# Performance work log

Hardware: AMD Instinct MI355X
Metric: run time of the kernel (lower is better)

## Reference

```python
import jax, jax.numpy as jnp
import numpy as np
import math

MODEL_DIM = 1024
B, S = 4, 2048


def setup_inputs() -> dict:
    key = jax.random.key(0)
    k_x, k_q, k_k, k_v = jax.random.split(key, 4)
    r5 = math.sqrt(5)
    x = jax.random.normal(k_x, (B, S, MODEL_DIM), dtype=jnp.float32)
    Q = jax.random.uniform(k_q, (MODEL_DIM, MODEL_DIM), minval=-r5, maxval=r5, dtype=jnp.float32)
    K = jax.random.uniform(k_k, (MODEL_DIM, MODEL_DIM), minval=-r5, maxval=r5, dtype=jnp.float32)
    V = jax.random.uniform(k_v, (MODEL_DIM, MODEL_DIM), minval=-r5, maxval=r5, dtype=jnp.float32)
    # attention_input == 'both' -> a == model_dim -> F is the full identity
    F = jnp.eye(MODEL_DIM, dtype=jnp.float32)
    return {"x": x, "Q": Q, "K": K, "V": V, "F": F}


def reference(x, Q, K, V, F):
    d = x.shape[-1]
    xf = jnp.matmul(x, F)
    Qx = jnp.matmul(xf, Q)          # [B,S,D]
    Kx = jnp.matmul(xf, K)          # [B,S,D]
    Vx = jnp.matmul(x, V)           # [B,S,D]
    scores = jnp.einsum('bqd,bkd->bqk', Qx, Kx) / math.sqrt(d)  # [B,S,S]
    seq = x.shape[1]
    mask = jnp.triu(jnp.ones((seq, seq), dtype=bool), k=1)
    scores = jnp.where(mask, -jnp.inf, scores)
    probs = jax.nn.softmax(scores, axis=-1)
    out = jnp.matmul(probs, Vx)     # [B,S,D]
    return (out, probs)
```

## Files before the change

kernel.cpp:

```cpp
#include <hip/hip_runtime.h>
#include <hip/hip_fp16.h>

typedef _Float16 f16;
typedef __attribute__((ext_vector_type(8))) _Float16 f16x8;
typedef __attribute__((ext_vector_type(4))) _Float16 f16x4;
typedef __attribute__((ext_vector_type(4))) float    f32x4;

#define D_MODEL 1024
#define SEQ     2048
#define BATCH   4
#define M_TOT   (BATCH * SEQ)
#define NE      ((long)M_TOT * D_MODEL)
#define WE      ((long)D_MODEL * D_MODEL)
#define OUT_ELEMS  ((long)M_TOT * D_MODEL)

static __device__ __forceinline__ f16x8 frag_read(const f16* lds, int row, int c)
{
    const f16x8* L = (const f16x8*)lds;
    return L[row * 4 + (c ^ ((row >> 1) & 3))];
}

static __device__ __forceinline__ void stage_tile(const f16* __restrict__ g, int row0,
                                                  int ld, int k0, f16* ldsbase,
                                                  int wave, int lane)
{
#pragma unroll
    for (int j = 0; j < 2; ++j) {
        const int chunk = wave * 2 + j;
        const int off16 = chunk * 64 + lane;
        const int row   = off16 >> 2;
        const int slot  = (off16 & 3) ^ ((row >> 1) & 3);
        const f16* src = g + (long)(row0 + row) * ld + (k0 + slot * 8);
        f16* dst = ldsbase + chunk * 512;
        __builtin_amdgcn_global_load_lds((const __attribute__((address_space(1))) void*)src,
                                         (__attribute__((address_space(3))) void*)dst,
                                         16, 0, 0);
    }
}

template<int ROWS>
static __device__ __forceinline__ void stage8(const f16* __restrict__ g, int row0,
                                              int ld, int k0, f16* dstbase,
                                              int wave, int lane)
{
#pragma unroll
    for (int j = 0; j < ROWS / 128; ++j) {
        const int off16 = j * 512 + wave * 64 + lane;
        const int row   = off16 >> 2;
        const int slot  = (off16 & 3) ^ ((row >> 1) & 3);
        const f16* src = g + (long)(row0 + row) * ld + (k0 + slot * 8);
        f16* dst = dstbase + (j * 512 + wave * 64) * 8;
        __builtin_amdgcn_global_load_lds((const __attribute__((address_space(1))) void*)src,
                                         (__attribute__((address_space(3))) void*)dst,
                                         16, 0, 0);
    }
}

template<int DUAL> struct G8 {
    static constexpr int BUF    = DUAL ? 24576 : 12288;
    static constexpr int OFF_AL = 8192;
    static constexpr int OFF_BH = DUAL ? 16384 : 8192;
    static constexpr int OFF_BL = 20480;
};

template<int DUAL>
static __device__ __forceinline__ void g8_issueA(const f16* Ah, const f16* Al, int ld,
                                                 int m0, f16* lds, int t, int wave, int lane)
{
    f16* b = lds + (t & 1) * G8<DUAL>::BUF;
    stage8<256>(Ah, m0, ld, t * 32, b, wave, lane);
    if constexpr (DUAL) stage8<256>(Al, m0, ld, t * 32, b + G8<DUAL>::OFF_AL, wave, lane);
}
template<int DUAL>
static __device__ __forceinline__ void g8_issueBh(const f16* BTh, int ld, int n0,
                                                  f16* lds, int t, int wave, int lane)
{
    stage8<128>(BTh, n0, ld, t * 32, lds + (t & 1) * G8<DUAL>::BUF + G8<DUAL>::OFF_BH, wave, lane);
}
template<int DUAL>
static __device__ __forceinline__ void g8_issueBl(const f16* BTl, int ld, int n0,
                                                  f16* lds, int t, int wave, int lane)
{
    stage8<128>(BTl, n0, ld, t * 32, lds + (t & 1) * G8<DUAL>::BUF + G8<DUAL>::OFF_BL, wave, lane);
}

template<int DUAL>
static __device__ __forceinline__ void gemm8_pipe(
    const f16* __restrict__ Ah, const f16* __restrict__ Al,
    const f16* __restrict__ BTh, const f16* __restrict__ BTl,
    int ld, int m0, int n0, int nT, f16* lds, f32x4 acc[4][4], int wave, int lane)
{
    const int wr = wave >> 1, wc = wave & 1;
    const int cf = lane >> 4;

#pragma unroll
    for (int mi = 0; mi < 4; ++mi)
#pragma unroll
        for (int ni = 0; ni < 4; ++ni) acc[mi][ni] = (f32x4){0.f, 0.f, 0.f, 0.f};

    g8_issueA<DUAL>(Ah, Al, ld, m0, lds, 0, wave, lane);
    g8_issueBh<DUAL>(BTh, ld, n0, lds, 0, wave, lane);
    if constexpr (DUAL) g8_issueBl<DUAL>(BTl, ld, n0, lds, 0, wave, lane);
    g8_issueA<DUAL>(Ah, Al, ld, m0, lds, 1, wave, lane);
    g8_issueBh<DUAL>(BTh, ld, n0, lds, 1, wave, lane);

    for (int t = 0; t < nT; ++t) {
        if (t < nT - 1) {
            if constexpr (DUAL) {
                g8_issueBl<DUAL>(BTl, ld, n0, lds, t + 1, wave, lane);
                asm volatile("s_waitcnt vmcnt(6)" ::: "memory");
            } else {
                asm volatile("s_waitcnt vmcnt(3)" ::: "memory");
            }
        } else {
            asm volatile("s_waitcnt vmcnt(0)" ::: "memory");
        }
        __builtin_amdgcn_sched_barrier(0);
        __builtin_amdgcn_s_barrier();
        __builtin_amdgcn_sched_barrier(0);

        f16* buf = lds + (t & 1) * G8<DUAL>::BUF;
        f16x8 fbh[4], fbl[4], fah[4], fal[4];
#pragma unroll
        for (int i = 0; i < 4; ++i) {
            const int rb = wc * 64 + i * 16 + (lane & 15);
            fbh[i] = frag_read(buf + G8<DUAL>::OFF_BH, rb, cf);
            if constexpr (DUAL) fbl[i] = frag_read(buf + G8<DUAL>::OFF_BL, rb, cf);
        }
#pragma unroll
        for (int i = 0; i < 4; ++i) {
            const int ra = wr * 64 + i * 16 + (lane & 15);
            fah[i] = frag_read(buf, ra, cf);
            if constexpr (DUAL) fal[i] = frag_read(buf + G8<DUAL>::OFF_AL, ra, cf);
        }

        if constexpr (DUAL) {
#pragma unroll
            for (int mi = 0; mi < 4; ++mi)
#pragma unroll
                for (int ni = 0; ni < 4; ++ni)
                    acc[mi][ni] = __builtin_amdgcn_mfma_f32_16x16x32_f16(fah[mi], fbh[ni], acc[mi][ni], 0, 0, 0);
        } else {
#pragma unroll
            for (int mi = 0; mi < 2; ++mi)
#pragma unroll
                for (int ni = 0; ni < 4; ++ni)
                    acc[mi][ni] = __builtin_amdgcn_mfma_f32_16x16x32_f16(fah[mi], fbh[ni], acc[mi][ni], 0, 0, 0);
        }

        asm volatile("s_waitcnt lgkmcnt(0)" ::: "memory");
        __builtin_amdgcn_sched_barrier(0);
        __builtin_amdgcn_s_barrier();
        __builtin_amdgcn_sched_barrier(0);

        if (t + 2 < nT) {
            g8_issueA<DUAL>(Ah, Al, ld, m0, lds, t + 2, wave, lane);
            g8_issueBh<DUAL>(BTh, ld, n0, lds, t + 2, wave, lane);
        }
        __builtin_amdgcn_sched_barrier(0);

        __builtin_amdgcn_s_setprio(1);
        if constexpr (DUAL) {
#pragma unroll
            for (int mi = 0; mi < 4; ++mi) {
#pragma unroll
                for (int ni = 0; ni < 4; ++ni)
                    acc[mi][ni] = __builtin_amdgcn_mfma_f32_16x16x32_f16(fah[mi], fbl[ni], acc[mi][ni], 0, 0, 0);
#pragma unroll
                for (int ni = 0; ni < 4; ++ni)
                    acc[mi][ni] = __builtin_amdgcn_mfma_f32_16x16x32_f16(fal[mi], fbh[ni], acc[mi][ni], 0, 0, 0);
            }
        } else {
#pragma unroll
            for (int mi = 2; mi < 4; ++mi)
#pragma unroll
                for (int ni = 0; ni < 4; ++ni)
                    acc[mi][ni] = __builtin_amdgcn_mfma_f32_16x16x32_f16(fah[mi], fbh[ni], acc[mi][ni], 0, 0, 0);
        }
        __builtin_amdgcn_s_setprio(0);
    }
}

#define BUFE2 32768

static __device__ __forceinline__ void g256_main(const f16* Ah, const f16* Al,
                                                 const f16* BTh, int ld, int m0, int n0,
                                                 f16* lds, int t, int wave, int lane)
{
    f16* b = lds + (t & 1) * BUFE2;
    stage8<256>(Ah,  m0, ld, t * 32, b,         wave, lane);
    stage8<256>(Al,  m0, ld, t * 32, b + 8192,  wave, lane);
    stage8<256>(BTh, n0, ld, t * 32, b + 16384, wave, lane);
}
static __device__ __forceinline__ void g256_bl(const f16* BTl, int ld, int n0,
                                               f16* lds, int t, int wave, int lane)
{
    stage8<256>(BTl, n0, ld, t * 32, lds + (t & 1) * BUFE2 + 24576, wave, lane);
}

static __device__ __forceinline__ void gemm256d(
    const f16* __restrict__ Ah, const f16* __restrict__ Al,
    const f16* __restrict__ BTh, const f16* __restrict__ BTl,
    int ld, int m0, int n0, f16* lds, f32x4 acc[8][4], int wave, int lane)
{
    const int wr = wave >> 2, wc = wave & 3;
    const int cf = lane >> 4;

#pragma unroll
    for (int mi = 0; mi < 8; ++mi)
#pragma unroll
        for (int ni = 0; ni < 4; ++ni) acc[mi][ni] = (f32x4){0.f, 0.f, 0.f, 0.f};

    g256_main(Ah, Al, BTh, ld, m0, n0, lds, 0, wave, lane);
    g256_bl(BTl, ld, n0, lds, 0, wave, lane);
    g256_main(Ah, Al, BTh, ld, m0, n0, lds, 1, wave, lane);

    for (int t = 0; t < 32; ++t) {
        if (t < 31) {
            g256_bl(BTl, ld, n0, lds, t + 1, wave, lane);
            asm volatile("s_waitcnt vmcnt(8)" ::: "memory");
        } else {
            asm volatile("s_waitcnt vmcnt(0)" ::: "memory");
        }
        __builtin_amdgcn_sched_barrier(0);
        __builtin_amdgcn_s_barrier();
        __builtin_amdgcn_sched_barrier(0);

        f16* buf = lds + (t & 1) * BUFE2;
        f16x8 fbh[4], fbl[4], fah[8], fal[8];
#pragma unroll
        for (int ni = 0; ni < 4; ++ni) {
            const int rb = wc * 64 + ni * 16 + (lane & 15);
            fbh[ni] = frag_read(buf + 16384, rb, cf);
            fbl[ni] = frag_read(buf + 24576, rb, cf);
        }
#pragma unroll
        for (int mi = 0; mi < 8; ++mi) {
            const int ra = wr * 128 + mi * 16 + (lane & 15);
            fah[mi] = frag_read(buf,        ra, cf);
            fal[mi] = frag_read(buf + 8192, ra, cf);
        }

#pragma unroll
        for (int mi = 0; mi < 8; ++mi)
#pragma unroll
            for (int ni = 0; ni < 4; ++ni)
                acc[mi][ni] = __builtin_amdgcn_mfma_f32_16x16x32_f16(fah[mi], fbh[ni], acc[mi][ni], 0, 0, 0);

        asm volatile("s_waitcnt lgkmcnt(0)" ::: "memory");
        __builtin_amdgcn_sched_barrier(0);
        __builtin_amdgcn_s_barrier();
        __builtin_amdgcn_sched_barrier(0);

        if (t < 30)
            g256_main(Ah, Al, BTh, ld, m0, n0, lds, t + 2, wave, lane);
        __builtin_amdgcn_sched_barrier(0);

        __builtin_amdgcn_s_setprio(1);
#pragma unroll
        for (int mi = 0; mi < 8; ++mi) {
#pragma unroll
            for (int ni = 0; ni < 4; ++ni)
                acc[mi][ni] = __builtin_amdgcn_mfma_f32_16x16x32_f16(fah[mi], fbl[ni], acc[mi][ni], 0, 0, 0);
#pragma unroll
            for (int ni = 0; ni < 4; ++ni)
                acc[mi][ni] = __builtin_amdgcn_mfma_f32_16x16x32_f16(fal[mi], fbh[ni], acc[mi][ni], 0, 0, 0);
        }
        __builtin_amdgcn_s_setprio(0);
    }
}

__global__ __launch_bounds__(512, 2) void k_gemm_T(
    const f16* __restrict__ xh, const f16* __restrict__ xl,
    const f16* __restrict__ WhT, const f16* __restrict__ WlT,
    f16* __restrict__ Th, f16* __restrict__ Tl)
{
    __shared__ __align__(16) f16 lds[49152];
    const int lane = threadIdx.x & 63, wave = threadIdx.x >> 6;
    const int L = blockIdx.x;
    const int swz = (L & 7) * 32 + (L >> 3);
    const int m0 = (swz >> 3) * 256;
    const int n0 = (swz & 7) * 128;
    f32x4 acc[4][4];
    gemm8_pipe<1>(xh, xl, WhT, WlT, D_MODEL, m0, n0, 32, lds, acc, wave, lane);
    const int wr = wave >> 1, wc = wave & 1;
#pragma unroll
    for (int mi = 0; mi < 4; ++mi)
#pragma unroll
        for (int ni = 0; ni < 4; ++ni) {
            const int gn = n0 + wc * 64 + ni * 16 + (lane & 15);
#pragma unroll
            for (int r = 0; r < 4; ++r) {
                const int gm = m0 + wr * 64 + mi * 16 + (lane >> 4) * 4 + r;
                const float v = acc[mi][ni][r];
                const f16 h = (f16)v;
                Th[(long)gm * D_MODEL + gn] = h;
                Tl[(long)gm * D_MODEL + gn] = (f16)(v - (float)h);
            }
        }
}

__global__ __launch_bounds__(512, 2) void k_mega1(
    const f16* __restrict__ Th, const f16* __restrict__ Tl,
    const f16* __restrict__ xh, const f16* __restrict__ xl,
    const f16* __restrict__ VhT,
    float* __restrict__ scores, f16* __restrict__ VxT)
{
    __shared__ __align__(16) f16 lds[65536];
    const int lane = threadIdx.x & 63, wave = threadIdx.x >> 6;

    if (blockIdx.x < 144) {
        const int L = blockIdx.x;
        const int b = L / 36;
        const int t = L - b * 36;
        int qt = (int)((sqrtf(8.f * (float)t + 1.f) - 1.f) * 0.5f);
        while ((qt + 1) * (qt + 2) / 2 <= t) ++qt;
        while (qt * (qt + 1) / 2 > t) --qt;
        const int kt = t - qt * (qt + 1) / 2;

        const long ob = (long)b * SEQ * D_MODEL;
        f32x4 acc[8][4];
        gemm256d(Th + ob, Tl + ob, xh + ob, xl + ob, D_MODEL,
                 qt * 256, kt * 256, lds, acc, wave, lane);

        float* sb = scores + (long)b * SEQ * SEQ;
        const int wr = wave >> 2, wc = wave & 3;
#pragma unroll
        for (int mi = 0; mi < 8; ++mi)
#pragma unroll
            for (int ni = 0; ni < 4; ++ni) {
                const int k = kt * 256 + wc * 64 + ni * 16 + (lane & 15);
#pragma unroll
                for (int r = 0; r < 4; ++r) {
                    const int q = qt * 256 + wr * 128 + mi * 16 + (lane >> 4) * 4 + r;
                    sb[(long)q * SEQ + k] = acc[mi][ni][r] * 0.03125f;
                }
            }
    } else {
        const int idx = blockIdx.x - 144;
        const int m0 = (idx >> 3) * 256;
        const int n0 = (idx & 7) * 128;
        f32x4 acc[4][4];
        gemm8_pipe<0>(xh, nullptr, VhT, nullptr, D_MODEL, m0, n0, 32, lds, acc, wave, lane);
        const int wr = wave >> 1, wc = wave & 1;
#pragma unroll
        for (int mi = 0; mi < 4; ++mi) {
            const int gm0 = m0 + wr * 64 + mi * 16 + (lane >> 4) * 4;
            const int b = gm0 >> 11, s = gm0 & 2047;
#pragma unroll
            for (int ni = 0; ni < 4; ++ni) {
                const int gn = n0 + wc * 64 + ni * 16 + (lane & 15);
                f16x4 p = {(f16)acc[mi][ni][0], (f16)acc[mi][ni][1],
                           (f16)acc[mi][ni][2], (f16)acc[mi][ni][3]};
                *(f16x4*)(VxT + ((long)b * D_MODEL + gn) * SEQ + s) = p;
            }
        }
    }
}

__global__ __launch_bounds__(512, 4) void k_gemm_pv8(
    const f16* __restrict__ P, const f16* __restrict__ VT, float* __restrict__ out)
{
    __shared__ __align__(16) f16 lds[24576];
    const int lane = threadIdx.x & 63, wave = threadIdx.x >> 6;
    const int i = blockIdx.x;
    const int qt = 7 - (i >> 5);
    const int dt = (i >> 2) & 7;
    const int b  = i & 3;
    const int nT = 8 * (qt + 1);
    f32x4 acc[4][4];
    const f16* Pb  = P  + (long)b * SEQ * SEQ;
    const f16* VTb = VT + (long)b * D_MODEL * SEQ;
    gemm8_pipe<0>(Pb, nullptr, VTb, nullptr, SEQ, qt * 256, dt * 128, nT, lds, acc, wave, lane);
    float* ob = out + (long)b * SEQ * D_MODEL;
    const int wr = wave >> 1, wc = wave & 1;
#pragma unroll
    for (int mi = 0; mi < 4; ++mi)
#pragma unroll
        for (int ni = 0; ni < 4; ++ni) {
            const int d = dt * 128 + wc * 64 + ni * 16 + (lane & 15);
#pragma unroll
            for (int r = 0; r < 4; ++r) {
                const int qq = qt * 256 + wr * 64 + mi * 16 + (lane >> 4) * 4 + r;
                ob[(long)qq * D_MODEL + d] = acc[mi][ni][r];
            }
        }
}

static __device__ __forceinline__ void gemm_core_dual(
    const f16* __restrict__ Ah, const f16* __restrict__ Al,
    const f16* __restrict__ BTh, const f16* __restrict__ BTl,
    int ld, int m0, int n0, int kEnd, f16* lds, f32x4 acc[4][4])
{
    const int t = threadIdx.x;
    const int lane = t & 63;
    const int wave = t >> 6;
    const int wr = wave >> 1, wc = wave & 1;
    const int cfrag = lane >> 4;

#pragma unroll
    for (int mi = 0; mi < 4; ++mi)
#pragma unroll
        for (int ni = 0; ni < 4; ++ni)
            acc[mi][ni] = (f32x4){0.f, 0.f, 0.f, 0.f};

    for (int k0 = 0; k0 < kEnd; k0 += 32) {
        stage_tile(Ah,  m0, ld, k0, lds,         wave, lane);
        stage_tile(BTh, n0, ld, k0, lds + 4096,  wave, lane);
        stage_tile(Al,  m0, ld, k0, lds + 8192,  wave, lane);
        stage_tile(BTl, n0, ld, k0, lds + 12288, wave, lane);
        __syncthreads();

        f16x8 fah[4], fbh[4], fal[4], fbl[4];
#pragma unroll
        for (int i = 0; i < 4; ++i) {
            fah[i] = frag_read(lds,         wr * 64 + i * 16 + (lane & 15), cfrag);
            fbh[i] = frag_read(lds + 4096,  wc * 64 + i * 16 + (lane & 15), cfrag);
            fal[i] = frag_read(lds + 8192,  wr * 64 + i * 16 + (lane & 15), cfrag);
            fbl[i] = frag_read(lds + 12288, wc * 64 + i * 16 + (lane & 15), cfrag);
        }
#pragma unroll
        for (int mi = 0; mi < 4; ++mi)
#pragma unroll
            for (int ni = 0; ni < 4; ++ni) {
                acc[mi][ni] = __builtin_amdgcn_mfma_f32_16x16x32_f16(fah[mi], fbh[ni], acc[mi][ni], 0, 0, 0);
                acc[mi][ni] = __builtin_amdgcn_mfma_f32_16x16x32_f16(fah[mi], fbl[ni], acc[mi][ni], 0, 0, 0);
                acc[mi][ni] = __builtin_amdgcn_mfma_f32_16x16x32_f16(fal[mi], fbh[ni], acc[mi][ni], 0, 0, 0);
            }
        __syncthreads();
    }
}

__global__ __launch_bounds__(256) void k_split_all(
    const float* __restrict__ x, const float* __restrict__ Q,
    const float* __restrict__ K, const float* __restrict__ V,
    f16* __restrict__ xh, f16* __restrict__ xl,
    f16* __restrict__ Qh, f16* __restrict__ Ql,
    f16* __restrict__ Kh, f16* __restrict__ Kl,
    f16* __restrict__ VhT)
{
    __shared__ float tile[32][33];
    const int bid = blockIdx.x;
    if (bid < 2560) {
        const float* src; f16 *dh, *dl; long base;
        if (bid < 2048)      { src = x; dh = xh; dl = xl; base = (long)bid * 4096; }
        else if (bid < 2304) { src = Q; dh = Qh; dl = Ql; base = (long)(bid - 2048) * 4096; }
        else                 { src = K; dh = Kh; dl = Kl; base = (long)(bid - 2304) * 4096; }
#pragma unroll
        for (int j = 0; j < 4; ++j) {
            const long i = base + (j * 256 + threadIdx.x) * 4;
            float4 v = *(const float4*)(src + i);
            f16 h0 = (f16)v.x, h1 = (f16)v.y, h2 = (f16)v.z, h3 = (f16)v.w;
            f16x4 hh = {h0, h1, h2, h3};
            f16x4 ll = {(f16)(v.x - (float)h0), (f16)(v.y - (float)h1),
                        (f16)(v.z - (float)h2), (f16)(v.w - (float)h3)};
            *(f16x4*)(dh + i) = hh;
            *(f16x4*)(dl + i) = ll;
        }
    } else {
        const int idx = bid - 2560;
        const int n0 = (idx & 31) * 32, k0 = (idx >> 5) * 32;
        const int c = threadIdx.x & 31, r8 = threadIdx.x >> 5;
#pragma unroll
        for (int i = 0; i < 4; ++i) {
            const int r = r8 + i * 8;
            tile[r][c] = V[(long)(k0 + r) * D_MODEL + n0 + c];
        }
        __syncthreads();
#pragma unroll
        for (int i = 0; i < 4; ++i) {
            const int r = r8 + i * 8;
            VhT[(long)(n0 + r) * D_MODEL + k0 + c] = (f16)tile[c][r];
        }
    }
}

__global__ __launch_bounds__(256, 2) void k_gemm_w(
    const f16* __restrict__ Qh, const f16* __restrict__ Ql,
    const f16* __restrict__ Kh, const f16* __restrict__ Kl,
    f16* __restrict__ WhT, f16* __restrict__ WlT)
{
    __shared__ __align__(16) f16 lds[16384];
    f32x4 acc[4][4];
    const int m0 = blockIdx.y * 128, n0 = blockIdx.x * 128;
    gemm_core_dual(Qh, Ql, Kh, Kl, D_MODEL, m0, n0, D_MODEL, lds, acc);
    const int lane = threadIdx.x & 63, wave = threadIdx.x >> 6;
    const int wr = wave >> 1, wc = wave & 1;
#pragma unroll
    for (int mi = 0; mi < 4; ++mi)
#pragma unroll
        for (int ni = 0; ni < 4; ++ni) {
            const int gn = n0 + wc * 64 + ni * 16 + (lane & 15);
#pragma unroll
            for (int r = 0; r < 4; ++r) {
                const int gm = m0 + wr * 64 + mi * 16 + (lane >> 4) * 4 + r;
                const float v = acc[mi][ni][r];
                const f16 h = (f16)v;
                WhT[(long)gn * D_MODEL + gm] = h;
                WlT[(long)gn * D_MODEL + gm] = (f16)(v - (float)h);
            }
        }
}

__global__ __launch_bounds__(256) void k_softmax(float* __restrict__ probs,
                                                 f16* __restrict__ probs16)
{
    const long row = blockIdx.x;
    const int q = (int)(row & (SEQ - 1));
    float* s = probs + row * SEQ;
    const int t = threadIdx.x;
    const int kb = t * 8;
    float v[8] = {0.f, 0.f, 0.f, 0.f, 0.f, 0.f, 0.f, 0.f};
    if (kb <= q) {
        float4 u0 = *(const float4*)(s + kb);
        float4 u1 = *(const float4*)(s + kb + 4);
        v[0] = u0.x; v[1] = u0.y; v[2] = u0.z; v[3] = u0.w;
        v[4] = u1.x; v[5] = u1.y; v[6] = u1.z; v[7] = u1.w;
    }
    float mx = -3.0e38f;
#pragma unroll
    for (int j = 0; j < 8; ++j) if (kb + j <= q) mx = fmaxf(mx, v[j]);
#pragma unroll
    for (int off = 32; off > 0; off >>= 1) mx = fmaxf(mx, __shfl_xor(mx, off, 64));
    __shared__ float redA[4], redB[4];
    const int lane = t & 63, wave = t >> 6;
    if (lane == 0) redA[wave] = mx;
    __syncthreads();
    mx = fmaxf(fmaxf(redA[0], redA[1]), fmaxf(redA[2], redA[3]));
    float e[8]; float sum = 0.f;
#pragma unroll
    for (int j = 0; j < 8; ++j) { e[j] = (kb + j <= q) ? __expf(v[j] - mx) : 0.f; sum += e[j]; }
#pragma unroll
    for (int off = 32; off > 0; off >>= 1) sum += __shfl_xor(sum, off, 64);
    if (lane == 0) redB[wave] = sum;
    __syncthreads();
    sum = (redB[0] + redB[1]) + (redB[2] + redB[3]);
    const float inv = 1.f / sum;
    f32x4 w0 = {e[0] * inv, e[1] * inv, e[2] * inv, e[3] * inv};
    f32x4 w1 = {e[4] * inv, e[5] * inv, e[6] * inv, e[7] * inv};
    __builtin_nontemporal_store(w0, (f32x4*)(s + kb));
    __builtin_nontemporal_store(w1, (f32x4*)(s + kb + 4));
    f16x8 p16 = {(f16)w0.x, (f16)w0.y, (f16)w0.z, (f16)w0.w,
                 (f16)w1.x, (f16)w1.y, (f16)w1.z, (f16)w1.w};
    *(f16x8*)(probs16 + row * SEQ + kb) = p16;
}

extern "C" void kernel_launch(void* const* d_in, const int* in_sizes, int n_in,
                              void* d_out, int out_size, void* d_ws, size_t ws_size,
                              hipStream_t stream)
{
    const float* x = (const float*)d_in[0];
    const float* Q = (const float*)d_in[1];
    const float* K = (const float*)d_in[2];
    const float* V = (const float*)d_in[3];

    float* out   = (float*)d_out;
    float* probs = out + OUT_ELEMS;

    f16* base = (f16*)d_ws;
    f16* xh   = base;
    f16* xl   = base + NE;
    f16* Th   = base + 2 * NE;
    f16* Tl   = base + 3 * NE;
    f16* VxT  = base + 4 * NE;
    f16* Qh   = base + 5 * NE;
    f16* Ql   = Qh + WE;
    f16* Kh   = Qh + 2 * WE;
    f16* Kl   = Qh + 3 * WE;
    f16* WhT  = Qh + 4 * WE;
    f16* WlT  = Qh + 5 * WE;
    f16* VhT  = Qh + 6 * WE;
    f16* probs16 = base + 2 * NE;

    k_split_all<<<3584, 256, 0, stream>>>(x, Q, K, V, xh, xl, Qh, Ql, Kh, Kl, VhT);
    k_gemm_w<<<dim3(8, 8), 256, 0, stream>>>(Qh, Ql, Kh, Kl, WhT, WlT);
    k_gemm_T<<<256, 512, 0, stream>>>(xh, xl, WhT, WlT, Th, Tl);
    k_mega1<<<400, 512, 0, stream>>>(Th, Tl, xh, xl, VhT, probs, VxT);
    k_softmax<<<8192, 256, 0, stream>>>(probs, probs16);
    k_gemm_pv8<<<256, 512, 0, stream>>>(probs16, VxT, out);
}
```

Baseline: 245.1 us.

## Rewrite Q·Kᵀ weight GEMM as split-K over waves with 64x64 tiles

Replaces the 64-block 128x128 weight-product GEMM with 256 blocks of 64x64 tiles, where each of the four waves handles a quarter of K in its own LDS region with no block-wide barriers. Partial sums are reduced through LDS, then split into hi/lo fp16 and transposed through LDS for vectorized coalesced stores. The goal is to fill more compute units and remove the scattered 2-byte transposed stores, at the cost of an extra LDS reduction and more LDS usage per block.

```diff
diff --git a/kernel.cpp b/kernel.cpp
--- a/kernel.cpp
+++ b/kernel.cpp
@@ -20,24 +20,6 @@
     return L[row * 4 + (c ^ ((row >> 1) & 3))];
 }
 
-static __device__ __forceinline__ void stage_tile(const f16* __restrict__ g, int row0,
-                                                  int ld, int k0, f16* ldsbase,
-                                                  int wave, int lane)
-{
-#pragma unroll
-    for (int j = 0; j < 2; ++j) {
-        const int chunk = wave * 2 + j;
-        const int off16 = chunk * 64 + lane;
-        const int row   = off16 >> 2;
-        const int slot  = (off16 & 3) ^ ((row >> 1) & 3);
-        const f16* src = g + (long)(row0 + row) * ld + (k0 + slot * 8);
-        f16* dst = ldsbase + chunk * 512;
-        __builtin_amdgcn_global_load_lds((const __attribute__((address_space(1))) void*)src,
-                                         (__attribute__((address_space(3))) void*)dst,
-                                         16, 0, 0);
-    }
-}
-
 template<int ROWS>
 static __device__ __forceinline__ void stage8(const f16* __restrict__ g, int row0,
                                               int ld, int k0, f16* dstbase,
@@ -50,6 +32,22 @@
         const int slot  = (off16 & 3) ^ ((row >> 1) & 3);
         const f16* src = g + (long)(row0 + row) * ld + (k0 + slot * 8);
         f16* dst = dstbase + (j * 512 + wave * 64) * 8;
+        __builtin_amdgcn_global_load_lds((const __attribute__((address_space(1))) void*)src,
+                                         (__attribute__((address_space(3))) void*)dst,
+                                         16, 0, 0);
+    }
+}
+
+static __device__ __forceinline__ void stage64(const f16* __restrict__ g, int row0,
+                                               int k0, f16* dstbase, int lane)
+{
+#pragma unroll
+    for (int j = 0; j < 4; ++j) {
+        const int off16 = j * 64 + lane;
+        const int row   = off16 >> 2;
+        const int slot  = (off16 & 3) ^ ((row >> 1) & 3);
+        const f16* src = g + (long)(row0 + row) * D_MODEL + (k0 + slot * 8);
+        f16* dst = dstbase + j * 512;
         __builtin_amdgcn_global_load_lds((const __attribute__((address_space(1))) void*)src,
                                          (__attribute__((address_space(3))) void*)dst,
                                          16, 0, 0);
@@ -387,37 +385,43 @@
         }
 }
 
-static __device__ __forceinline__ void gemm_core_dual(
-    const f16* __restrict__ Ah, const f16* __restrict__ Al,
-    const f16* __restrict__ BTh, const f16* __restrict__ BTl,
-    int ld, int m0, int n0, int kEnd, f16* lds, f32x4 acc[4][4])
-{
-    const int t = threadIdx.x;
-    const int lane = t & 63;
-    const int wave = t >> 6;
-    const int wr = wave >> 1, wc = wave & 1;
-    const int cfrag = lane >> 4;
-
+__global__ __launch_bounds__(256) void k_gemm_w64(
+    const f16* __restrict__ Qh, const f16* __restrict__ Ql,
+    const f16* __restrict__ Kh, const f16* __restrict__ Kl,
+    f16* __restrict__ WhT, f16* __restrict__ WlT)
+{
+    __shared__ __align__(16) f16 lds[36864];
+    const int tid  = threadIdx.x;
+    const int lane = tid & 63, wave = tid >> 6;
+    const int m0 = (blockIdx.x >> 4) * 64;
+    const int n0 = (blockIdx.x & 15) * 64;
+    const int cf = lane >> 4;
+
+    f16* wb = lds + wave * 8192;
+    f32x4 acc[4][4];
 #pragma unroll
     for (int mi = 0; mi < 4; ++mi)
 #pragma unroll
-        for (int ni = 0; ni < 4; ++ni)
-            acc[mi][ni] = (f32x4){0.f, 0.f, 0.f, 0.f};
-
-    for (int k0 = 0; k0 < kEnd; k0 += 32) {
-        stage_tile(Ah,  m0, ld, k0, lds,         wave, lane);
-        stage_tile(BTh, n0, ld, k0, lds + 4096,  wave, lane);
-        stage_tile(Al,  m0, ld, k0, lds + 8192,  wave, lane);
-        stage_tile(BTl, n0, ld, k0, lds + 12288, wave, lane);
-        __syncthreads();
-
-        f16x8 fah[4], fbh[4], fal[4], fbl[4];
+        for (int ni = 0; ni < 4; ++ni) acc[mi][ni] = (f32x4){0.f, 0.f, 0.f, 0.f};
+
+    const int kw = wave * 256;
+    for (int s = 0; s < 8; ++s) {
+        const int k0 = kw + s * 32;
+        stage64(Qh, m0, k0, wb,        lane);
+        stage64(Ql, m0, k0, wb + 2048, lane);
+        stage64(Kh, n0, k0, wb + 4096, lane);
+        stage64(Kl, n0, k0, wb + 6144, lane);
+        asm volatile("s_waitcnt vmcnt(0)" ::: "memory");
+        __builtin_amdgcn_sched_barrier(0);
+
+        f16x8 fah[4], fal[4], fbh[4], fbl[4];
 #pragma unroll
         for (int i = 0; i < 4; ++i) {
-            fah[i] = frag_read(lds,         wr * 64 + i * 16 + (lane & 15), cfrag);
-            fbh[i] = frag_read(lds + 4096,  wc * 64 + i * 16 + (lane & 15), cfrag);
-            fal[i] = frag_read(lds + 8192,  wr * 64 + i * 16 + (lane & 15), cfrag);
-            fbl[i] = frag_read(lds + 12288, wc * 64 + i * 16 + (lane & 15), cfrag);
+            const int r = i * 16 + (lane & 15);
+            fah[i] = frag_read(wb,        r, cf);
+            fal[i] = frag_read(wb + 2048, r, cf);
+            fbh[i] = frag_read(wb + 4096, r, cf);
+            fbl[i] = frag_read(wb + 6144, r, cf);
         }
 #pragma unroll
         for (int mi = 0; mi < 4; ++mi)
@@ -427,7 +431,54 @@
                 acc[mi][ni] = __builtin_amdgcn_mfma_f32_16x16x32_f16(fah[mi], fbl[ni], acc[mi][ni], 0, 0, 0);
                 acc[mi][ni] = __builtin_amdgcn_mfma_f32_16x16x32_f16(fal[mi], fbh[ni], acc[mi][ni], 0, 0, 0);
             }
-        __syncthreads();
+        asm volatile("s_waitcnt lgkmcnt(0)" ::: "memory");
+        __builtin_amdgcn_sched_barrier(0);
+    }
+
+    __syncthreads();
+    float* lf = (float*)lds;
+#pragma unroll
+    for (int mi = 0; mi < 4; ++mi)
+#pragma unroll
+        for (int ni = 0; ni < 4; ++ni)
+#pragma unroll
+            for (int r = 0; r < 4; ++r) {
+                const int row = mi * 16 + (lane >> 4) * 4 + r;
+                const int col = ni * 16 + (lane & 15);
+                lf[wave * 4096 + row * 64 + col] = acc[mi][ni][r];
+            }
+    __syncthreads();
+
+    const int row = tid >> 2;
+    const int c0  = (tid & 3) * 16;
+    float vsum[16];
+#pragma unroll
+    for (int j = 0; j < 16; ++j) {
+        const int idx = row * 64 + c0 + j;
+        vsum[j] = (lf[idx] + lf[4096 + idx]) + (lf[8192 + idx] + lf[12288 + idx]);
+    }
+    __syncthreads();
+
+    f16* th = lds;
+    f16* tl = lds + 4224;
+#pragma unroll
+    for (int j = 0; j < 16; ++j) {
+        const f16 h = (f16)vsum[j];
+        th[(c0 + j) * 66 + row] = h;
+        tl[(c0 + j) * 66 + row] = (f16)(vsum[j] - (float)h);
+    }
+    __syncthreads();
+
+    const int c  = tid >> 2;
+    const int r0 = (tid & 3) * 16;
+    f16 oh[16], ol[16];
+#pragma unroll
+    for (int j = 0; j < 16; ++j) { oh[j] = th[c * 66 + r0 + j]; ol[j] = tl[c * 66 + r0 + j]; }
+    long gbase = (long)(n0 + c) * D_MODEL + m0 + r0;
+#pragma unroll
+    for (int j = 0; j < 2; ++j) {
+        *(f16x8*)(WhT + gbase + j * 8) = *(f16x8*)(oh + j * 8);
+        *(f16x8*)(WlT + gbase + j * 8) = *(f16x8*)(ol + j * 8);
     }
 }
 
@@ -473,33 +524,6 @@
             VhT[(long)(n0 + r) * D_MODEL + k0 + c] = (f16)tile[c][r];
         }
     }
-}
-
-__global__ __launch_bounds__(256, 2) void k_gemm_w(
-    const f16* __restrict__ Qh, const f16* __restrict__ Ql,
-    const f16* __restrict__ Kh, const f16* __restrict__ Kl,
-    f16* __restrict__ WhT, f16* __restrict__ WlT)
-{
-    __shared__ __align__(16) f16 lds[16384];
-    f32x4 acc[4][4];
-    const int m0 = blockIdx.y * 128, n0 = blockIdx.x * 128;
-    gemm_core_dual(Qh, Ql, Kh, Kl, D_MODEL, m0, n0, D_MODEL, lds, acc);
-    const int lane = threadIdx.x & 63, wave = threadIdx.x >> 6;
-    const int wr = wave >> 1, wc = wave & 1;
-#pragma unroll
-    for (int mi = 0; mi < 4; ++mi)
-#pragma unroll
-        for (int ni = 0; ni < 4; ++ni) {
-            const int gn = n0 + wc * 64 + ni * 16 + (lane & 15);
-#pragma unroll
-            for (int r = 0; r < 4; ++r) {
-                const int gm = m0 + wr * 64 + mi * 16 + (lane >> 4) * 4 + r;
-                const float v = acc[mi][ni][r];
-                const f16 h = (f16)v;
-                WhT[(long)gn * D_MODEL + gm] = h;
-                WlT[(long)gn * D_MODEL + gm] = (f16)(v - (float)h);
-            }
-        }
 }
 
 __global__ __launch_bounds__(256) void k_softmax(float* __restrict__ probs,
@@ -573,7 +597,7 @@
     f16* probs16 = base + 2 * NE;
 
     k_split_all<<<3584, 256, 0, stream>>>(x, Q, K, V, xh, xl, Qh, Ql, Kh, Kl, VhT);
-    k_gemm_w<<<dim3(8, 8), 256, 0, stream>>>(Qh, Ql, Kh, Kl, WhT, WlT);
+    k_gemm_w64<<<256, 256, 0, stream>>>(Qh, Ql, Kh, Kl, WhT, WlT);
     k_gemm_T<<<256, 512, 0, stream>>>(xh, xl, WhT, WlT, Th, Tl);
     k_mega1<<<400, 512, 0, stream>>>(Th, Tl, xh, xl, VhT, probs, VxT);
     k_softmax<<<8192, 256, 0, stream>>>(probs, probs16);
```

Result: faster. 228.8 us (-6.6%).
